# Kernel optimization log

Measured on AMD Instinct MI355X. Metric: run time of the kernel, lower is better.

## Reference

```python
import jax, jax.numpy as jnp
import numpy as np


def _conv(x, w):
    # SpykeTorch snn.Convolution: plain conv2d, no bias, no padding (VALID)
    return jax.lax.conv_general_dilated(
        x, w, window_strides=(1, 1), padding='VALID',
        dimension_numbers=('NCHW', 'OIHW', 'NCHW'))


def _pad2(x, p=2):
    # sf.pad(input, pad=(2,2,2,2), value=0): zero-pad last two (spatial) dims
    return jnp.pad(x, ((0, 0), (0, 0), (p, p), (p, p)))


def _fire(pot, thr):
    # sf.fire: thresholded[pot <= thr] = 0 ; spk = thresholded.sign()
    thresholded = jnp.where(pot > thr, pot, jnp.zeros((), pot.dtype))
    spk = (pot > thr).astype(pot.dtype)
    return spk, thresholded


def _pool(x, k, s):
    # sf.pooling: max_pool2d, floor mode (== VALID reduce_window)
    return jax.lax.reduce_window(
        x, -jnp.inf, jax.lax.max,
        window_dimensions=(1, 1, k, k),
        window_strides=(1, 1, s, s),
        padding='VALID')


def setup_inputs() -> dict:
    key = jax.random.key(0)
    kx, k1, k2, k3 = jax.random.split(key, 4)
    # (T, C, H, W): T timesteps act as batch in SpykeTorch
    x = jax.random.uniform(kx, (20, 6, 160, 160), dtype=jnp.float32)

    def xavier_normal(k, shape):
        fan_in = shape[1] * shape[2] * shape[3]
        fan_out = shape[0] * shape[2] * shape[3]
        std = float(np.sqrt(2.0 / (fan_in + fan_out)))
        return jax.random.normal(k, shape, dtype=jnp.float32) * std

    w1 = xavier_normal(k1, (30, 6, 4, 4))
    w2 = xavier_normal(k2, (250, 30, 3, 3))
    w3 = xavier_normal(k3, (200, 250, 3, 3))
    return {'x': x, 'w1': w1, 'w2': w2, 'w3': w3, 'layer_idx': 3}


def reference(x, w1, w2, w3, layer_idx):
    # Eval-mode forward path of deepSNN up to `layer_idx` (tensor-returning branches)
    CONV1_T, CONV2_T, CONV3_T = 1.0, 1.0, 25.0
    inp = _pad2(x.astype(jnp.float32))          # (T,6,164,164)
    pot = _conv(inp, w1)                        # (T,30,161,161)
    spk, pot = _fire(pot, CONV1_T)
    if layer_idx == 1:
        return spk, pot
    pot = _conv(_pad2(_pool(spk, 2, 2)), w2)    # (T,250,82,82)
    spk, pot = _fire(pot, CONV2_T)
    if layer_idx == 2:
        return spk, pot
    pot = _conv(_pad2(_pool(spk, 3, 3)), w3)    # (T,200,29,29)
    spk, pot = _fire(pot, CONV3_T)
    return spk, pot
```

## Files before the change

kernel.cpp:

```cpp
#include <hip/hip_runtime.h>
#include <hip/hip_bf16.h>
#include <hip/hip_fp16.h>


#define OUT_HALF 3364000
#define MASK_PLANE 128000
#define T_FLOATS 168200

typedef float f32x16 __attribute__((ext_vector_type(16)));
typedef short bf8s __attribute__((ext_vector_type(8)));
typedef float f32x4 __attribute__((ext_vector_type(4)));
typedef float v2f __attribute__((ext_vector_type(2)));
typedef f32x4 f32x4u __attribute__((aligned(4)));

static __device__ __forceinline__ unsigned int pkbf(float a, float b) {
    union { __hip_bfloat162 h; unsigned int u; } cv;
    cv.h = __float22bfloat162_rn(make_float2(a, b));
    return cv.u;
}
static __device__ __forceinline__ unsigned short bfbits(float a) {
    union { __hip_bfloat16 h; unsigned short u; } cv;
    cv.h = __float2bfloat16(a);
    return cv.u;
}
static __device__ __forceinline__ v2f up2(unsigned int u) {
    union { unsigned int u32; __half2 h2; } cv; cv.u32 = u;
    float2 f = __half22float2(cv.h2);
    v2f r; r.x = f.x; r.y = f.y;
    return r;
}
static __device__ __forceinline__ unsigned long long expand32(unsigned int v) {
    unsigned long long x = v;
    x = (x | (x << 16)) & 0x0000FFFF0000FFFFull;
    x = (x | (x << 8))  & 0x00FF00FF00FF00FFull;
    x = (x | (x << 4))  & 0x0F0F0F0F0F0F0F0Full;
    x = (x | (x << 2))  & 0x3333333333333333ull;
    x = (x | (x << 1))  & 0x5555555555555555ull;
    return x;
}

__global__ __launch_bounds__(256) void k_prep(const float* __restrict__ x,
                                              const float* __restrict__ w2,
                                              float* __restrict__ xpad,
                                              unsigned int* __restrict__ w2h,
                                              unsigned int* __restrict__ flags2) {
    int bidx = blockIdx.x;
    int tid = threadIdx.x;
    if (bidx >= 1576) {
        int tb = bidx - 1576;
        if (tb == 0)
            for (int i = tid; i < 540; i += 256) flags2[i] = 0u;
        int idx = tb * 256 + tid;
        if (idx < 34560) {
            int ck = idx >> 7, pl = idx & 127;
            int oc0 = 2 * pl, oc1 = oc0 + 1;
            float a = (oc0 < 250) ? w2[oc0 * 270 + ck] : 0.f;
            float b = (oc1 < 250) ? w2[oc1 * 270 + ck] : 0.f;
            union { __half2 h2; unsigned int u; } cv;
            cv.h2.x = __float2half(a);
            cv.h2.y = __float2half(b);
            w2h[idx] = cv.u;
        }
        return;
    }
    for (int e = bidx * 256 + tid; e < 3227520; e += 403456) {
        int tc = e / 26896;
        int rem = e - tc * 26896;
        int r = rem / 164, col = rem - r * 164;
        int sr = r - 2, sc = col - 2;
        float v = 0.f;
        if ((unsigned)sr < 160u && (unsigned)sc < 160u)
            v = x[(tc * 160 + sr) * 160 + sc];
        xpad[e] = v;
    }
}

__global__ __launch_bounds__(256) void k_conv1m(const float* __restrict__ xpad,
                                                const float* __restrict__ w1,
                                                unsigned int* __restrict__ mask1) {
    __shared__ unsigned short B_lds[6 * 64 * 8];

    int tid = threadIdx.x;
#pragma unroll
    for (int n = 0; n < 12; ++n) {
        int q = n * 256 + tid;
        int i = q & 7, ll = (q >> 3) & 63, ks = q >> 9;
        int oc = ll & 31;
        int kg = ks * 16 + ((ll >> 5) << 3) + i;
        float w = (oc < 30) ? w1[oc * 96 + kg] : 0.f;
        B_lds[q] = bfbits(w);
    }
    __syncthreads();

    int l = tid & 63, wv = tid >> 6;
    int b = blockIdx.x;
    int t = b / 100;
    int u = (b % 100) * 4 + wv;
    int pr = u / 5, jblk = u % 5;
    int m = l & 31, hi = l >> 5;
    int j = jblk * 32 + m;

    bf8s bq[6];
#pragma unroll
    for (int ks = 0; ks < 6; ++ks)
        bq[ks] = *(const bf8s*)&B_lds[(ks * 64 + l) * 8];

    f32x16 acc0 = (f32x16)(0.0f);
    f32x16 acc1 = (f32x16)(0.0f);
    int r0 = 2 * pr + 2 * hi;

#pragma unroll
    for (int ks = 0; ks < 6; ++ks) {
        const float* base = xpad + ((t * 6 + ks) * 164 + r0) * 164 + j;
        f32x4 v0 = *(const f32x4u*)(base);
        f32x4 v1 = *(const f32x4u*)(base + 164);
        f32x4 v2 = *(const f32x4u*)(base + 328);
        union { bf8s s; unsigned int u4[4]; } a0, a1;
        a0.u4[0] = pkbf(v0.x, v0.y);
        a0.u4[1] = pkbf(v0.z, v0.w);
        a0.u4[2] = pkbf(v1.x, v1.y);
        a0.u4[3] = pkbf(v1.z, v1.w);
        a1.u4[0] = a0.u4[2];
        a1.u4[1] = a0.u4[3];
        a1.u4[2] = pkbf(v2.x, v2.y);
        a1.u4[3] = pkbf(v2.z, v2.w);
        acc0 = __builtin_amdgcn_mfma_f32_32x32x16_bf16(a0.s, bq[ks], acc0, 0, 0, 0);
        acc1 = __builtin_amdgcn_mfma_f32_32x32x16_bf16(a1.s, bq[ks], acc1, 0, 0, 0);
    }

    unsigned int mbase = (unsigned int)((t * 80 + pr) * 80 + jblk * 16);
#pragma unroll
    for (int a = 0; a < 8; ++a) {
        bool s = acc0[2 * a] > 1.f || acc0[2 * a + 1] > 1.f ||
                 acc1[2 * a] > 1.f || acc1[2 * a + 1] > 1.f;
        unsigned long long bal = __ballot(s);
        if (l < 6) {
            int h = l >> 1;
            unsigned int word = (l & 1) ? (unsigned int)(bal >> 32)
                                        : (unsigned int)bal;
            int pc = (a & 1) + ((a >> 1) << 2) + ((l & 1) << 1);
            mask1[h * MASK_PLANE + mbase + pc] = (word >> (10 * h)) & 0x3FFu;
        }
    }
}

__global__ __launch_bounds__(256) void k_conv2(const unsigned int* __restrict__ mask1,
                                               const unsigned int* __restrict__ w2h,
                                               unsigned long long* __restrict__ pool2m,
                                               unsigned int* __restrict__ flags2) {
    __shared__ unsigned int m_lds[5 * 84];
    __shared__ int f2;

    int b = blockIdx.x;
    int ninth = b % 9;  b /= 9;
    int ph = b % 27;
    int t = b / 27;
    int tid = threadIdx.x;
    int l = tid & 63, wv = tid >> 6;
    int h = wv & 1, grp = wv >> 1;
    int r0 = 3 * ph - 2;
    int pwA = ninth * 3;

    if (tid == 0) f2 = 0;
    for (int idx = tid; idx < 420; idx += 256) {
        int r = idx / 84, col = idx % 84;
        int gr = r0 + r, gc = col - 2;
        unsigned int v = 0;
        if ((unsigned)gr < 80u && (unsigned)gc < 80u) {
            int i2 = (t * 80 + gr) * 80 + gc;
            v = mask1[i2] | (mask1[MASK_PLANE + i2] << 10) |
                (mask1[2 * MASK_PLANE + i2] << 20);
        }
        m_lds[idx] = v;
    }
    __syncthreads();

    const unsigned int* wb = w2h + h * 64 + l;
    unsigned long long* prow = pool2m + ((t * 27 + ph) * 27) * 4 + 2 * h;
    v2f z2 = (v2f)(0.f);

    if (grp == 0) {
        int c0A = 3 * pwA, c0B = c0A + 3;
        unsigned int qA[25], qB[25];
#pragma unroll
        for (int dr = 0; dr < 5; ++dr)
#pragma unroll
            for (int ds = 0; ds < 5; ++ds) {
                qA[dr * 5 + ds] = m_lds[dr * 84 + c0A + ds];
                qB[dr * 5 + ds] = m_lds[dr * 84 + c0B + ds];
            }

        v2f accA[3][3], accB[3][3];
#pragma unroll
        for (int i = 0; i < 3; ++i)
#pragma unroll
            for (int j = 0; j < 3; ++j) { accA[i][j] = z2; accB[i][j] = z2; }

#pragma unroll
        for (int dr = 0; dr < 5; ++dr) {
#pragma unroll
            for (int ds = 0; ds < 5; ++ds) {
                unsigned int mA = qA[dr * 5 + ds];
                unsigned int mB = qB[dr * 5 + ds];
                while (mA | mB) {
                    bool hA = mA != 0, hB = mB != 0;
                    int cA = __builtin_ctz(mA | 0x40000000u);
                    int cB = __builtin_ctz(mB | 0x40000000u);
                    mA &= mA - 1;
                    mB &= mB - 1;
                    const unsigned int* pA = wb + cA * 1152;
                    const unsigned int* pB = wb + cB * 1152;
                    unsigned int uA[3][3], uB[3][3];
#pragma unroll
                    for (int i = 0; i < 3; ++i) {
                        if (dr - i < 0 || dr - i > 2) continue;
#pragma unroll
                        for (int j = 0; j < 3; ++j) {
                            if (ds - j < 0 || ds - j > 2) continue;
                            int off = ((dr - i) * 3 + (ds - j)) * 128;
                            uA[i][j] = pA[off];
                            uB[i][j] = pB[off];
                        }
                    }
#pragma unroll
                    for (int i = 0; i < 3; ++i) {
                        if (dr - i < 0 || dr - i > 2) continue;
#pragma unroll
                        for (int j = 0; j < 3; ++j) {
                            if (ds - j < 0 || ds - j > 2) continue;
                            accA[i][j] += hA ? up2(uA[i][j]) : z2;
                            accB[i][j] += hB ? up2(uB[i][j]) : z2;
                        }
                    }
                }
            }
        }

        bool sA0 = false, sA1 = false, sB0 = false, sB1 = false;
#pragma unroll
        for (int i = 0; i < 3; ++i)
#pragma unroll
            for (int j = 0; j < 3; ++j) {
                sA0 = sA0 || (accA[i][j].x > 1.f);
                sA1 = sA1 || (accA[i][j].y > 1.f);
                sB0 = sB0 || (accB[i][j].x > 1.f);
                sB1 = sB1 || (accB[i][j].y > 1.f);
            }
        unsigned long long bA0 = __ballot(sA0), bA1 = __ballot(sA1);
        unsigned long long bB0 = __ballot(sB0), bB1 = __ballot(sB1);
        unsigned long long wA0 = expand32((unsigned int)bA0) |
                                 (expand32((unsigned int)bA1) << 1);
        unsigned long long wA1 = expand32((unsigned int)(bA0 >> 32)) |
                                 (expand32((unsigned int)(bA1 >> 32)) << 1);
        unsigned long long wB0 = expand32((unsigned int)bB0) |
                                 (expand32((unsigned int)bB1) << 1);
        unsigned long long wB1 = expand32((unsigned int)(bB0 >> 32)) |
                                 (expand32((unsigned int)(bB1 >> 32)) << 1);
        if (l == 0) {
            prow[pwA * 4]           = wA0;
            prow[pwA * 4 + 1]       = wA1;
            prow[(pwA + 1) * 4]     = wB0;
            prow[(pwA + 1) * 4 + 1] = wB1;
        }
        if (wA0 | wA1 | wB0 | wB1) f2 = 1;
    } else {
        int pw = pwA + 2;
        int c0 = 3 * pw;
        unsigned int q[25];
#pragma unroll
        for (int dr = 0; dr < 5; ++dr)
#pragma unroll
            for (int ds = 0; ds < 5; ++ds)
                q[dr * 5 + ds] = m_lds[dr * 84 + c0 + ds];

        v2f acc[3][3];
#pragma unroll
        for (int i = 0; i < 3; ++i)
#pragma unroll
            for (int j = 0; j < 3; ++j) acc[i][j] = z2;

#pragma unroll
        for (int dr = 0; dr < 5; ++dr) {
#pragma unroll
            for (int ds = 0; ds < 5; ++ds) {
                unsigned int m = q[dr * 5 + ds];
                while (m) {
                    int c1 = __builtin_ctz(m); m &= m - 1;
                    bool has2 = (m != 0);
                    int c2 = c1;
                    if (has2) { c2 = __builtin_ctz(m); m &= m - 1; }
                    const unsigned int* p1 = wb + c1 * 1152;
                    const unsigned int* p2 = wb + c2 * 1152;
                    unsigned int u1[3][3], u2[3][3];
#pragma unroll
                    for (int i = 0; i < 3; ++i) {
                        if (dr - i < 0 || dr - i > 2) continue;
#pragma unroll
                        for (int j = 0; j < 3; ++j) {
                            if (ds - j < 0 || ds - j > 2) continue;
                            int off = ((dr - i) * 3 + (ds - j)) * 128;
                            u1[i][j] = p1[off];
                            u2[i][j] = p2[off];
                        }
                    }
#pragma unroll
                    for (int i = 0; i < 3; ++i) {
                        if (dr - i < 0 || dr - i > 2) continue;
#pragma unroll
                        for (int j = 0; j < 3; ++j) {
                            if (ds - j < 0 || ds - j > 2) continue;
                            acc[i][j] += up2(u1[i][j]);
                            acc[i][j] += has2 ? up2(u2[i][j]) : z2;
                        }
                    }
                }
            }
        }

        bool s0 = false, s1 = false;
#pragma unroll
        for (int i = 0; i < 3; ++i)
#pragma unroll
            for (int j = 0; j < 3; ++j) {
                s0 = s0 || (acc[i][j].x > 1.f);
                s1 = s1 || (acc[i][j].y > 1.f);
            }
        unsigned long long b0 = __ballot(s0), b1 = __ballot(s1);
        unsigned long long w0 = expand32((unsigned int)b0) |
                                (expand32((unsigned int)b1) << 1);
        unsigned long long w1 = expand32((unsigned int)(b0 >> 32)) |
                                (expand32((unsigned int)(b1 >> 32)) << 1);
        if (l == 0) {
            prow[pw * 4]     = w0;
            prow[pw * 4 + 1] = w1;
        }
        if (w0 | w1) f2 = 1;
    }

    __syncthreads();
    if (tid == 0 && f2) flags2[t * 27 + ph] = 1u;
}

__global__ __launch_bounds__(320) void k_conv3(const unsigned long long* __restrict__ pool2m,
                                               const float* __restrict__ w3,
                                               float* __restrict__ out,
                                               const unsigned int* __restrict__ flags2) {
    __shared__ float w_lds[25 * 9 * 40];
    __shared__ float in_lds[25 * 4 * 34];

    int b = blockIdx.x;
    int rb = b % 15;  b /= 15;
    int ocg = b % 5;  b /= 5;
    int t = b;
    int oc0 = ocg * 40;
    int r0 = 2 * rb;
    int tid = threadIdx.x;
    int ocl = tid % 40, ct = tid / 40;

    {
        unsigned int fT = 0;
        const unsigned int* fp = flags2 + t * 27;
#pragma unroll
        for (int r = 0; r < 27; ++r) fT |= fp[r];
        if (fT == 0) {
            float4 z; z.x = 0.f; z.y = 0.f; z.z = 0.f; z.w = 0.f;
            float4* o0 = (float4*)(out + (size_t)t * T_FLOATS);
            float4* o1 = (float4*)(out + OUT_HALF + (size_t)t * T_FLOATS);
            int s = ocg * 15 + rb;
            int lo = s * 561;
            int hi = lo + 561; if (hi > 42050) hi = 42050;
            for (int i = lo + tid; i < hi; i += 320) {
                o0[i] = z;
                o1[i] = z;
            }
            return;
        }
    }

    {
        unsigned int f = 0;
        int rlo = r0 - 2; if (rlo < 0) rlo = 0;
        int rhi = r0 + 1; if (rhi > 26) rhi = 26;
        for (int r = rlo; r <= rhi; ++r) f |= flags2[t * 27 + r];
        if (f == 0) {
            int nrows = (r0 + 1 < 29) ? 2 : 1;
            int stride = 29 * nrows;
            int cnt = 40 * stride;
            for (int idx = tid; idx < cnt; idx += 320) {
                int o = idx / stride, rem = idx % stride;
                size_t base = (size_t)((t * 200 + oc0 + o) * 29 + r0) * 29 + rem;
                out[base] = 0.f;
                out[OUT_HALF + base] = 0.f;
            }
            return;
        }
    }

    float acc[2][4];
#pragma unroll
    for (int i = 0; i < 2; ++i)
#pragma unroll
        for (int j = 0; j < 4; ++j) acc[i][j] = 0.f;

    for (int chn = 0; chn < 10; ++chn) {
        int cc0 = chn * 25;
        for (int idx = tid; idx < 25 * 9 * 40; idx += 320) {
            int o = idx % 40, ck = idx / 40;
            int ckg = cc0 * 9 + ck;
            w_lds[idx] = w3[(size_t)(oc0 + o) * 2250 + ckg];
        }
        for (int idx = tid; idx < 25 * 4 * 34; idx += 320) {
            int col = idx % 34;
            int rem = idx / 34;
            int r = rem & 3, cl = rem >> 2;
            int gr = r0 + r - 2, gc = col - 2;
            float v = 0.f;
            if ((unsigned)gr < 27u && (unsigned)gc < 27u) {
                int c = cc0 + cl;
                unsigned long long wbits =
                    pool2m[((t * 27 + gr) * 27 + gc) * 4 + (c >> 6)];
                v = (float)((wbits >> (c & 63)) & 1ull);
            }
            in_lds[idx] = v;
        }
        __syncthreads();

        for (int cl = 0; cl < 25; ++cl) {
            float in[4][6];
#pragma unroll
            for (int r = 0; r < 4; ++r)
#pragma unroll
                for (int j = 0; j < 6; ++j)
                    in[r][j] = in_lds[(cl * 4 + r) * 34 + ct * 4 + j];
            const float* wp = &w_lds[cl * 360 + ocl];
#pragma unroll
            for (int k = 0; k < 9; ++k) {
                float w = wp[k * 40];
                int kh = k / 3, kw = k % 3;
#pragma unroll
                for (int i = 0; i < 2; ++i)
#pragma unroll
                    for (int j = 0; j < 4; ++j)
                        acc[i][j] += in[i + kh][j + kw] * w;
            }
        }
        __syncthreads();
    }

    {
        int oc = oc0 + ocl;
#pragma unroll
        for (int i = 0; i < 2; ++i) {
            int r = r0 + i;
            if (r < 29) {
#pragma unroll
                for (int j = 0; j < 4; ++j) {
                    int col = ct * 4 + j;
                    if (col < 29) {
                        float pot = acc[i][j];
                        bool s = pot > 25.f;
                        size_t base = ((size_t)((t * 200 + oc) * 29 + r)) * 29 + col;
                        out[base] = s ? 1.f : 0.f;
                        out[OUT_HALF + base] = s ? pot : 0.f;
                    }
                }
            }
        }
    }
}

extern "C" void kernel_launch(void* const* d_in, const int* in_sizes, int n_in,
                              void* d_out, int out_size, void* d_ws, size_t ws_size,
                              hipStream_t stream) {
    const float* x  = (const float*)d_in[0];
    const float* w1 = (const float*)d_in[1];
    const float* w2 = (const float*)d_in[2];
    const float* w3 = (const float*)d_in[3];
    float* out = (float*)d_out;

    unsigned int* mask1 = (unsigned int*)d_ws;
    unsigned long long* pool2m = (unsigned long long*)((char*)d_ws + 1536000);
    unsigned int* w2h = (unsigned int*)((char*)d_ws + 2002560);
    unsigned int* flags2 = (unsigned int*)((char*)d_ws + 2277376);
    float* xpad = (float*)((char*)d_ws + 4194304);

    k_prep<<<1711, 256, 0, stream>>>(x, w2, xpad, w2h, flags2);
    k_conv1m<<<2000, 256, 0, stream>>>(xpad, w1, mask1);
    k_conv2<<<20 * 27 * 9, 256, 0, stream>>>(mask1, w2h, pool2m, flags2);
    k_conv3<<<20 * 5 * 15, 320, 0, stream>>>(pool2m, w3, out, flags2);
}
```

Baseline: 126.2 us.

## Fuse input padding into conv1 and drop block-level flag sync in conv2

Removes the separate prep kernel that materialised a zero-padded copy of the input. Conv1 now reads the raw input directly, using a fast vector-load path for interior tiles and a bounds-checked scalar path at the borders. The w2 fp16 packing and flag clearing move into extra blocks of the conv1 launch. Conv2 writes its per-row flag directly from each wave instead of going through a shared variable and a trailing __syncthreads. This saves one kernel launch and a full read and write of the padded input, at the cost of some branch divergence at the edges. It also relies on the flag clear in the extra conv1 blocks finishing before conv2 runs, which stream ordering guarantees.

```diff
diff --git a/kernel.cpp b/kernel.cpp
--- a/kernel.cpp
+++ b/kernel.cpp
@@ -39,48 +39,31 @@
     return x;
 }
 
-__global__ __launch_bounds__(256) void k_prep(const float* __restrict__ x,
-                                              const float* __restrict__ w2,
-                                              float* __restrict__ xpad,
-                                              unsigned int* __restrict__ w2h,
-                                              unsigned int* __restrict__ flags2) {
-    int bidx = blockIdx.x;
+__global__ __launch_bounds__(256) void k_conv1m(const float* __restrict__ x,
+                                                const float* __restrict__ w1,
+                                                const float* __restrict__ w2,
+                                                unsigned int* __restrict__ w2h,
+                                                unsigned int* __restrict__ mask1,
+                                                unsigned int* __restrict__ flags2) {
     int tid = threadIdx.x;
-    if (bidx >= 1576) {
-        int tb = bidx - 1576;
+    if (blockIdx.x >= 2000) {
+        int tb = blockIdx.x - 2000;
         if (tb == 0)
             for (int i = tid; i < 540; i += 256) flags2[i] = 0u;
         int idx = tb * 256 + tid;
-        if (idx < 34560) {
-            int ck = idx >> 7, pl = idx & 127;
-            int oc0 = 2 * pl, oc1 = oc0 + 1;
-            float a = (oc0 < 250) ? w2[oc0 * 270 + ck] : 0.f;
-            float b = (oc1 < 250) ? w2[oc1 * 270 + ck] : 0.f;
-            union { __half2 h2; unsigned int u; } cv;
-            cv.h2.x = __float2half(a);
-            cv.h2.y = __float2half(b);
-            w2h[idx] = cv.u;
-        }
+        int ck = idx >> 7, pl = idx & 127;
+        int oc0 = 2 * pl, oc1 = oc0 + 1;
+        float a = (oc0 < 250) ? w2[oc0 * 270 + ck] : 0.f;
+        float bb = (oc1 < 250) ? w2[oc1 * 270 + ck] : 0.f;
+        union { __half2 h2; unsigned int u; } cv;
+        cv.h2.x = __float2half(a);
+        cv.h2.y = __float2half(bb);
+        w2h[idx] = cv.u;
         return;
     }
-    for (int e = bidx * 256 + tid; e < 3227520; e += 403456) {
-        int tc = e / 26896;
-        int rem = e - tc * 26896;
-        int r = rem / 164, col = rem - r * 164;
-        int sr = r - 2, sc = col - 2;
-        float v = 0.f;
-        if ((unsigned)sr < 160u && (unsigned)sc < 160u)
-            v = x[(tc * 160 + sr) * 160 + sc];
-        xpad[e] = v;
-    }
-}
-
-__global__ __launch_bounds__(256) void k_conv1m(const float* __restrict__ xpad,
-                                                const float* __restrict__ w1,
-                                                unsigned int* __restrict__ mask1) {
+
     __shared__ unsigned short B_lds[6 * 64 * 8];
 
-    int tid = threadIdx.x;
 #pragma unroll
     for (int n = 0; n < 12; ++n) {
         int q = n * 256 + tid;
@@ -107,14 +90,33 @@
 
     f32x16 acc0 = (f32x16)(0.0f);
     f32x16 acc1 = (f32x16)(0.0f);
-    int r0 = 2 * pr + 2 * hi;
+    int sr0 = 2 * pr + 2 * hi - 2;
+    int sc0 = j - 2;
+    bool fast = ((unsigned)sr0 <= 157u) && ((unsigned)sc0 <= 156u);
 
 #pragma unroll
     for (int ks = 0; ks < 6; ++ks) {
-        const float* base = xpad + ((t * 6 + ks) * 164 + r0) * 164 + j;
-        f32x4 v0 = *(const f32x4u*)(base);
-        f32x4 v1 = *(const f32x4u*)(base + 164);
-        f32x4 v2 = *(const f32x4u*)(base + 328);
+        const float* xp = x + (t * 6 + ks) * 25600;
+        f32x4 v0, v1, v2;
+        if (fast) {
+            const float* bp = xp + sr0 * 160 + sc0;
+            v0 = *(const f32x4u*)(bp);
+            v1 = *(const f32x4u*)(bp + 160);
+            v2 = *(const f32x4u*)(bp + 320);
+        } else {
+            float tmp[3][4];
+#pragma unroll
+            for (int r = 0; r < 3; ++r)
+#pragma unroll
+                for (int e = 0; e < 4; ++e) {
+                    int sr = sr0 + r, sc = sc0 + e;
+                    tmp[r][e] = ((unsigned)sr < 160u && (unsigned)sc < 160u)
+                                    ? xp[sr * 160 + sc] : 0.f;
+                }
+            v0.x = tmp[0][0]; v0.y = tmp[0][1]; v0.z = tmp[0][2]; v0.w = tmp[0][3];
+            v1.x = tmp[1][0]; v1.y = tmp[1][1]; v1.z = tmp[1][2]; v1.w = tmp[1][3];
+            v2.x = tmp[2][0]; v2.y = tmp[2][1]; v2.z = tmp[2][2]; v2.w = tmp[2][3];
+        }
         union { bf8s s; unsigned int u4[4]; } a0, a1;
         a0.u4[0] = pkbf(v0.x, v0.y);
         a0.u4[1] = pkbf(v0.z, v0.w);
@@ -149,7 +151,6 @@
                                                unsigned long long* __restrict__ pool2m,
                                                unsigned int* __restrict__ flags2) {
     __shared__ unsigned int m_lds[5 * 84];
-    __shared__ int f2;
 
     int b = blockIdx.x;
     int ninth = b % 9;  b /= 9;
@@ -161,7 +162,6 @@
     int r0 = 3 * ph - 2;
     int pwA = ninth * 3;
 
-    if (tid == 0) f2 = 0;
     for (int idx = tid; idx < 420; idx += 256) {
         int r = idx / 84, col = idx % 84;
         int gr = r0 + r, gc = col - 2;
@@ -262,7 +262,8 @@
             prow[(pwA + 1) * 4]     = wB0;
             prow[(pwA + 1) * 4 + 1] = wB1;
         }
-        if (wA0 | wA1 | wB0 | wB1) f2 = 1;
+        if ((wA0 | wA1 | wB0 | wB1) && l == 0)
+            flags2[t * 27 + ph] = 1u;
     } else {
         int pw = pwA + 2;
         int c0 = 3 * pw;
@@ -334,11 +335,8 @@
             prow[pw * 4]     = w0;
             prow[pw * 4 + 1] = w1;
         }
-        if (w0 | w1) f2 = 1;
-    }
-
-    __syncthreads();
-    if (tid == 0 && f2) flags2[t * 27 + ph] = 1u;
+        if ((w0 | w1) && l == 0) flags2[t * 27 + ph] = 1u;
+    }
 }
 
 __global__ __launch_bounds__(320) void k_conv3(const unsigned long long* __restrict__ pool2m,
@@ -482,10 +480,8 @@
     unsigned long long* pool2m = (unsigned long long*)((char*)d_ws + 1536000);
     unsigned int* w2h = (unsigned int*)((char*)d_ws + 2002560);
     unsigned int* flags2 = (unsigned int*)((char*)d_ws + 2277376);
-    float* xpad = (float*)((char*)d_ws + 4194304);
-
-    k_prep<<<1711, 256, 0, stream>>>(x, w2, xpad, w2h, flags2);
-    k_conv1m<<<2000, 256, 0, stream>>>(xpad, w1, mask1);
+
+    k_conv1m<<<2135, 256, 0, stream>>>(x, w1, w2, w2h, mask1, flags2);
     k_conv2<<<20 * 27 * 9, 256, 0, stream>>>(mask1, w2h, pool2m, flags2);
     k_conv3<<<20 * 5 * 15, 320, 0, stream>>>(pool2m, w3, out, flags2);
 }
```

Measured after the change: 124.9 us. Within noise of the previous version (-1.0%).
